# Kernel tuning notes

Hardware: AMD Instinct MI355X
Metric: run time of the kernel (lower is better)

The kernel has to match this reference:

```python
import jax, jax.numpy as jnp
import numpy as np

H = 128        # hidden_dim
NP = 512       # program nodes
NV = 50000     # voxel nodes
E = 800000     # cross edges (16 per voxel)
TAU = 1.0
SLOPE = 0.01   # LeakyReLU default negative slope


def setup_inputs() -> dict:
    key = jax.random.key(0)
    ks = jax.random.split(key, 12)
    s = 1.0 / np.sqrt(H)
    x = jax.random.normal(ks[0], (NP, H), dtype=jnp.float32)
    v = jax.random.normal(ks[1], (NV, H), dtype=jnp.float32)
    row0 = jax.random.randint(ks[2], (E,), 0, NP, dtype=jnp.int32)
    row1 = (jnp.arange(E, dtype=jnp.int32) % NV)  # every voxel gets E/NV edges
    cross_edge_index = jnp.stack([row0, row1])    # [2, E]
    W_program = jax.random.normal(ks[3], (H, H), dtype=jnp.float32) * s
    b_program = jnp.zeros((H,), dtype=jnp.float32)
    W_voxel = jax.random.normal(ks[4], (H, H), dtype=jnp.float32) * s
    b_voxel = jnp.zeros((H,), dtype=jnp.float32)
    W_m1 = jax.random.normal(ks[5], (H, H), dtype=jnp.float32) * s
    b_m1 = jnp.zeros((H,), dtype=jnp.float32)
    W_m2 = jax.random.normal(ks[6], (H, 1), dtype=jnp.float32) * s
    b_m2 = jnp.zeros((1,), dtype=jnp.float32)
    theta = jax.random.normal(ks[7], (H, 1), dtype=jnp.float32) * s  # xavier-like
    u = jax.random.uniform(ks[8], (E,), dtype=jnp.float32)
    gumbel_u = jnp.clip(u, 1e-7, 1.0 - 1e-7)  # avoid log(0)
    return {"x": x, "v": v, "cross_edge_index": cross_edge_index,
            "W_program": W_program, "b_program": b_program,
            "W_voxel": W_voxel, "b_voxel": b_voxel,
            "W_m1": W_m1, "b_m1": b_m1, "W_m2": W_m2, "b_m2": b_m2,
            "theta": theta, "gumbel_u": gumbel_u}


def reference(x, v, cross_edge_index, W_program, b_program, W_voxel, b_voxel,
              W_m1, b_m1, W_m2, b_m2, theta, gumbel_u):
    src = cross_edge_index[0]
    dst = cross_edge_index[1]
    x_sel = x[src]                      # [E, H] gather
    v_sel = v[dst]                      # [E, H] gather
    # mask = sigmoid(MLP(v)) : Linear -> LeakyReLU -> Linear(H,1)
    a = v @ W_m1 + b_m1
    a = jnp.where(a >= 0, a, SLOPE * a)
    mask = jax.nn.sigmoid(a @ W_m2 + b_m2)                  # [NV, 1]
    # attention logits: theta^T * tanh(Wp x_sel + Wv v_sel), summed over H
    t = jnp.tanh(x_sel @ W_program + b_program + v_sel @ W_voxel + b_voxel)
    e = jnp.sum(t * theta[:, 0], axis=-1)                   # [E]
    # Gumbel softmax: global softmax over all edges (dim=0 in torch on 1-D e)
    g = -jnp.log(-jnp.log(gumbel_u))
    y = jax.nn.softmax((e + g) / TAU)                       # [E]
    # per-voxel hard argmax (scatter_max), straight-through estimator
    seg_max = jax.ops.segment_max(y, dst, num_segments=NV)  # [NV]
    is_max = y == seg_max[dst]
    cand = jnp.where(is_max, jnp.arange(E), E)
    argmax = jax.ops.segment_min(cand, dst, num_segments=NV)  # [NV], first max per voxel
    y_hard_1 = jnp.zeros(E + 1, y.dtype).at[argmax].set(1.0)[:E]  # overflow slot for empty segments
    y_hard = jax.lax.stop_gradient(y_hard_1 - y) + y
    # scatter-sum of soft-attended program features back to voxels
    summed = jax.ops.segment_sum(x_sel * y[:, None], dst, num_segments=NV)  # [NV, H]
    v_out = v + mask * summed
    return (v_out, mask, y[:, None], y_hard[:, None])
```

## Files before the change

### kernel.cpp

```cpp
#include <hip/hip_runtime.h>

#define H     128
#define NP    512
#define NVOX  50000
#define NEDGE 800000
#define EPV   16
#define SLOPE 0.01f
#define GR    32
#define NBLK  ((NVOX + GR - 1) / GR)
#define STRH  136
#define VSTR  132
#define C1    2.8853900817779268f
#define LOG2E 1.4426950408889634f
#define LN2   0.6931471805599453f

#define EXP2(x) __builtin_amdgcn_exp2f(x)
#define LOG2(x) __builtin_amdgcn_logf(x)
#define RCP(x)  __builtin_amdgcn_rcpf(x)

typedef _Float16 h16;
typedef __attribute__((ext_vector_type(4))) _Float16 h16x4;
typedef __attribute__((ext_vector_type(8))) _Float16 h16x8;
typedef __attribute__((ext_vector_type(4))) float    f32x4;

__global__ __launch_bounds__(256) void k_pre(const float* __restrict__ x,
                                             const float* __restrict__ Wp,
                                             const float* __restrict__ bp,
                                             const float* __restrict__ Wv,
                                             const float* __restrict__ Wm1,
                                             float* __restrict__ xpout,
                                             h16* __restrict__ WvThi,
                                             h16* __restrict__ WvTlo,
                                             h16* __restrict__ Wm1T) {
    __shared__ float part[H];
    int bid = blockIdx.x;
    int tid = threadIdx.x;
    if (bid < NP) {
        int row = bid;
        int col = tid & 127;
        int kh  = tid >> 7;
        int kbase = kh * 64;
        const float* xr = x + (size_t)row * H;
        float acc = 0.f;
#pragma unroll 8
        for (int k = 0; k < 64; ++k)
            acc = fmaf(xr[kbase + k], Wp[(size_t)(kbase + k) * H + col], acc);
        if (kh == 1) part[col] = acc;
        __syncthreads();
        if (kh == 0) xpout[(size_t)row * H + col] = (acc + part[col] + bp[col]) * C1;
    } else {
        int idx = (bid - NP) * 256 + tid;
        if (idx < 16384) {
            int k = idx >> 7, n = idx & 127;
            float w = Wv[idx];
            h16 hi = (h16)w;
            WvThi[n * H + k] = hi;
            WvTlo[n * H + k] = (h16)(w - (float)hi);
        } else {
            int j = idx - 16384;
            int k = j >> 7, n = j & 127;
            Wm1T[n * H + k] = (h16)Wm1[j];
        }
    }
}

__global__ __launch_bounds__(256) void k_main(
    const float* __restrict__ v,
    const float* __restrict__ bv,  const float* __restrict__ bm1,
    const float* __restrict__ Wm2, const float* __restrict__ bm2,
    const h16* __restrict__ WvThi, const h16* __restrict__ WvTlo,
    const h16* __restrict__ Wm1T,
    const float* __restrict__ xp,  const int* __restrict__ cei,
    const float* __restrict__ theta, const float* __restrict__ gum,
    float* __restrict__ mask_out, float* __restrict__ pout,
    float* __restrict__ partial)
{
    __shared__ __align__(16) char ldsbuf[GR * STRH * 2 * 2];
    h16*   vh = (h16*)ldsbuf;
    h16*   vl = vh + GR * STRH;
    float* vt = (float*)ldsbuf;
    __shared__ float pmbuf[4][GR];
    __shared__ float psums[4];

    int tid  = threadIdx.x;
    int base = blockIdx.x * GR;

#pragma unroll
    for (int i = 0; i < 4; ++i) {
        int f  = i * 256 + tid;
        int r  = f >> 5, c4 = f & 31;
        int gr = base + r;
        float4 val = (gr < NVOX) ? *(const float4*)&v[(size_t)gr * H + c4 * 4]
                                 : make_float4(0.f, 0.f, 0.f, 0.f);
        h16x4 hi, lo;
        hi.x = (h16)val.x; lo.x = (h16)(val.x - (float)hi.x);
        hi.y = (h16)val.y; lo.y = (h16)(val.y - (float)hi.y);
        hi.z = (h16)val.z; lo.z = (h16)(val.z - (float)hi.z);
        hi.w = (h16)val.w; lo.w = (h16)(val.w - (float)hi.w);
        *(h16x4*)&vh[r * STRH + c4 * 4] = hi;
        *(h16x4*)&vl[r * STRH + c4 * 4] = lo;
    }
    __syncthreads();

    int wave = tid >> 6, lane = tid & 63;
    int m16 = lane & 15, quad = lane >> 4;
    int cb = wave * 32;

    f32x4 aV[2][2], aM[2][2];
#pragma unroll
    for (int rt = 0; rt < 2; ++rt)
#pragma unroll
        for (int ct = 0; ct < 2; ++ct) { aV[rt][ct] = (f32x4)0.f; aM[rt][ct] = (f32x4)0.f; }

#pragma unroll
    for (int kc = 0; kc < 4; ++kc) {
        int kofs = kc * 32 + quad * 8;
        h16x8 ah[2], al[2];
#pragma unroll
        for (int rt = 0; rt < 2; ++rt) {
            int row = rt * 16 + m16;
            ah[rt] = *(const h16x8*)&vh[row * STRH + kofs];
            al[rt] = *(const h16x8*)&vl[row * STRH + kofs];
        }
#pragma unroll
        for (int ct = 0; ct < 2; ++ct) {
            int n = cb + ct * 16 + m16;
            h16x8 bh = *(const h16x8*)&WvThi[n * H + kofs];
            h16x8 bl = *(const h16x8*)&WvTlo[n * H + kofs];
            h16x8 bm = *(const h16x8*)&Wm1T[n * H + kofs];
#pragma unroll
            for (int rt = 0; rt < 2; ++rt) {
                aV[rt][ct] = __builtin_amdgcn_mfma_f32_16x16x32_f16(ah[rt], bh, aV[rt][ct], 0, 0, 0);
                aV[rt][ct] = __builtin_amdgcn_mfma_f32_16x16x32_f16(al[rt], bh, aV[rt][ct], 0, 0, 0);
                aV[rt][ct] = __builtin_amdgcn_mfma_f32_16x16x32_f16(ah[rt], bl, aV[rt][ct], 0, 0, 0);
                aM[rt][ct] = __builtin_amdgcn_mfma_f32_16x16x32_f16(ah[rt], bm, aM[rt][ct], 0, 0, 0);
            }
        }
    }
    __syncthreads();

    float pml[2][4];
#pragma unroll
    for (int rt = 0; rt < 2; ++rt)
#pragma unroll
        for (int reg = 0; reg < 4; ++reg) pml[rt][reg] = 0.f;
#pragma unroll
    for (int ct = 0; ct < 2; ++ct) {
        int col = cb + ct * 16 + m16;
        float bvc = bv[col], bmc = bm1[col], w2c = Wm2[col];
#pragma unroll
        for (int rt = 0; rt < 2; ++rt)
#pragma unroll
            for (int reg = 0; reg < 4; ++reg) {
                int row = rt * 16 + quad * 4 + reg;
                vt[row * VSTR + col] = (aV[rt][ct][reg] + bvc) * C1;
                float m = aM[rt][ct][reg] + bmc;
                m = (m >= 0.f) ? m : SLOPE * m;
                pml[rt][reg] = fmaf(m, w2c, pml[rt][reg]);
            }
    }
#pragma unroll
    for (int off = 8; off >= 1; off >>= 1)
#pragma unroll
        for (int rt = 0; rt < 2; ++rt)
#pragma unroll
            for (int reg = 0; reg < 4; ++reg)
                pml[rt][reg] += __shfl_xor(pml[rt][reg], off, 64);
    if (m16 == 0) {
#pragma unroll
        for (int rt = 0; rt < 2; ++rt)
#pragma unroll
            for (int reg = 0; reg < 4; ++reg)
                pmbuf[wave][rt * 16 + quad * 4 + reg] = pml[rt][reg];
    }
    __syncthreads();
    if (wave == 0 && lane < GR) {
        int gr = base + lane;
        if (gr < NVOX) {
            float s = pmbuf[0][lane] + pmbuf[1][lane] + pmbuf[2][lane]
                    + pmbuf[3][lane] + bm2[0];
            mask_out[gr] = RCP(1.f + EXP2(-s * LOG2E));
        }
    }

    int g = tid >> 3, lk = tid & 7;
    float th2[16], thsum = 0.f;
#pragma unroll
    for (int i = 0; i < 4; ++i) {
        float4 t4 = *(const float4*)&theta[(lk + 8 * i) * 4];
        th2[i * 4 + 0] = -2.f * t4.x; th2[i * 4 + 1] = -2.f * t4.y;
        th2[i * 4 + 2] = -2.f * t4.z; th2[i * 4 + 3] = -2.f * t4.w;
        thsum += t4.x + t4.y + t4.z + t4.w;
    }
    int vox = base + g;
    bool valid = vox < NVOX;
    const float* vr = &vt[g * VSTR];
    float4 b0 = *(const float4*)&vr[(lk +  0) * 4];
    float4 b1 = *(const float4*)&vr[(lk +  8) * 4];
    float4 b2 = *(const float4*)&vr[(lk + 16) * 4];
    float4 b3 = *(const float4*)&vr[(lk + 24) * 4];

    float psum = 0.f;
    for (int t = 0; t < EPV; ++t) {
        int e   = vox + t * NVOX;
        int src = valid ? cei[e] : 0;
        const float4* xr = (const float4*)(xp + (size_t)src * H);
        float4 a0 = xr[lk], a1 = xr[lk + 8], a2 = xr[lk + 16], a3 = xr[lk + 24];
        float acc0 = thsum, acc1 = 0.f;
        acc0 = fmaf(th2[ 0], RCP(EXP2(a0.x + b0.x) + 1.f), acc0);
        acc1 = fmaf(th2[ 1], RCP(EXP2(a0.y + b0.y) + 1.f), acc1);
        acc0 = fmaf(th2[ 2], RCP(EXP2(a0.z + b0.z) + 1.f), acc0);
        acc1 = fmaf(th2[ 3], RCP(EXP2(a0.w + b0.w) + 1.f), acc1);
        acc0 = fmaf(th2[ 4], RCP(EXP2(a1.x + b1.x) + 1.f), acc0);
        acc1 = fmaf(th2[ 5], RCP(EXP2(a1.y + b1.y) + 1.f), acc1);
        acc0 = fmaf(th2[ 6], RCP(EXP2(a1.z + b1.z) + 1.f), acc0);
        acc1 = fmaf(th2[ 7], RCP(EXP2(a1.w + b1.w) + 1.f), acc1);
        acc0 = fmaf(th2[ 8], RCP(EXP2(a2.x + b2.x) + 1.f), acc0);
        acc1 = fmaf(th2[ 9], RCP(EXP2(a2.y + b2.y) + 1.f), acc1);
        acc0 = fmaf(th2[10], RCP(EXP2(a2.z + b2.z) + 1.f), acc0);
        acc1 = fmaf(th2[11], RCP(EXP2(a2.w + b2.w) + 1.f), acc1);
        acc0 = fmaf(th2[12], RCP(EXP2(a3.x + b3.x) + 1.f), acc0);
        acc1 = fmaf(th2[13], RCP(EXP2(a3.y + b3.y) + 1.f), acc1);
        acc0 = fmaf(th2[14], RCP(EXP2(a3.z + b3.z) + 1.f), acc0);
        acc1 = fmaf(th2[15], RCP(EXP2(a3.w + b3.w) + 1.f), acc1);
        float acc = acc0 + acc1;
        acc += __shfl_xor(acc, 4, 64);
        acc += __shfl_xor(acc, 2, 64);
        acc += __shfl_xor(acc, 1, 64);
        if (lk == 0 && valid) {
            float u  = gum[e];
            float l1 = LOG2(u);
            float t1 = -LN2 * l1;
            float gm = -LN2 * LOG2(t1);
            float p  = EXP2((acc + gm) * LOG2E);
            pout[e] = p;
            psum   += p;
        }
    }
#pragma unroll
    for (int off = 32; off >= 1; off >>= 1) psum += __shfl_xor(psum, off, 64);
    __syncthreads();
    if (lane == 0) psums[wave] = psum;
    __syncthreads();
    if (tid == 0)
        partial[blockIdx.x] = psums[0] + psums[1] + psums[2] + psums[3];
}

__global__ __launch_bounds__(256) void k_reduce(const float* __restrict__ partial,
                                                float* __restrict__ invS) {
    __shared__ float wsum[4];
    int tid = threadIdx.x;
    float s = 0.f;
    for (int i = tid; i < NBLK; i += 256) s += partial[i];
#pragma unroll
    for (int off = 32; off >= 1; off >>= 1) s += __shfl_xor(s, off, 64);
    if ((tid & 63) == 0) wsum[tid >> 6] = s;
    __syncthreads();
    if (tid == 0) invS[0] = 1.f / (wsum[0] + wsum[1] + wsum[2] + wsum[3]);
}

__global__ __launch_bounds__(256) void k_out(const float* __restrict__ v,
                                             const float* __restrict__ x,
                                             const int* __restrict__ cei,
                                             const float* __restrict__ maskp,
                                             const float* __restrict__ invSp,
                                             float* __restrict__ vout,
                                             float* __restrict__ ybuf,
                                             float* __restrict__ yhard) {
    __shared__ float yt[EPV][32];
    __shared__ int   st[EPV][32];
    __shared__ int   am[32];
    int tid  = threadIdx.x;
    int base = blockIdx.x * 32;
    float invS = invSp[0];
#pragma unroll
    for (int it = 0; it < 2; ++it) {
        int idx = it * 256 + tid;
        int t = idx >> 5, c = idx & 31;
        int vox = base + c;
        if (vox < NVOX) {
            int e = vox + t * NVOX;
            float y = ybuf[e] * invS;
            yt[t][c] = y;
            st[t][c] = cei[e];
            ybuf[e]  = y;
        }
    }
    __syncthreads();
    if (tid < 32 && base + tid < NVOX) {
        int c = tid;
        float mx = yt[0][c]; int a = 0;
#pragma unroll
        for (int t = 1; t < EPV; ++t) {
            float yv = yt[t][c];
            if (yv > mx) { mx = yv; a = t; }
        }
        am[c] = a;
    }
    __syncthreads();
#pragma unroll
    for (int it = 0; it < 2; ++it) {
        int idx = it * 256 + tid;
        int t = idx >> 5, c = idx & 31;
        int vox = base + c;
        if (vox < NVOX) yhard[vox + t * NVOX] = (t == am[c]) ? 1.f : 0.f;
    }
    int c4 = (tid & 31) * 4;
    for (int vx = tid >> 5; vx < 32; vx += 8) {
        int vox = base + vx;
        if (vox >= NVOX) break;
        float4 acc = make_float4(0.f, 0.f, 0.f, 0.f);
#pragma unroll
        for (int t = 0; t < EPV; ++t) {
            float y = yt[t][vx];
            const float4 xv = *(const float4*)&x[(size_t)st[t][vx] * H + c4];
            acc.x = fmaf(y, xv.x, acc.x);
            acc.y = fmaf(y, xv.y, acc.y);
            acc.z = fmaf(y, xv.z, acc.z);
            acc.w = fmaf(y, xv.w, acc.w);
        }
        float m = maskp[vox];
        const float4 vv = *(const float4*)&v[(size_t)vox * H + c4];
        float4 o;
        o.x = fmaf(m, acc.x, vv.x);
        o.y = fmaf(m, acc.y, vv.y);
        o.z = fmaf(m, acc.z, vv.z);
        o.w = fmaf(m, acc.w, vv.w);
        *(float4*)&vout[(size_t)vox * H + c4] = o;
    }
}

extern "C" void kernel_launch(void* const* d_in, const int* in_sizes, int n_in,
                              void* d_out, int out_size, void* d_ws, size_t ws_size,
                              hipStream_t stream) {
    (void)in_sizes; (void)n_in; (void)out_size; (void)ws_size;
    const float* x   = (const float*)d_in[0];
    const float* v   = (const float*)d_in[1];
    const int*   cei = (const int*)d_in[2];
    const float* Wp  = (const float*)d_in[3];
    const float* bp  = (const float*)d_in[4];
    const float* Wv  = (const float*)d_in[5];
    const float* bv  = (const float*)d_in[6];
    const float* Wm1 = (const float*)d_in[7];
    const float* bm1 = (const float*)d_in[8];
    const float* Wm2 = (const float*)d_in[9];
    const float* bm2 = (const float*)d_in[10];
    const float* th  = (const float*)d_in[11];
    const float* gum = (const float*)d_in[12];

    float* out   = (float*)d_out;
    float* vout  = out;
    float* maskp = out + (size_t)NVOX * H;
    float* ybuf  = maskp + NVOX;
    float* yhard = ybuf + NEDGE;
    float* xp      = yhard;
    float* partial = yhard + 65536;
    h16*   WvThi   = (h16*)(yhard + 67104);
    h16*   WvTlo   = WvThi + 16384;
    h16*   Wm1T    = WvThi + 32768;
    float* invS    = (float*)d_ws;

    k_pre<<<NP + 128, 256, 0, stream>>>(x, Wp, bp, Wv, Wm1, xp, WvThi, WvTlo, Wm1T);
    k_main<<<NBLK, 256, 0, stream>>>(v, bv, bm1, Wm2, bm2, WvThi, WvTlo, Wm1T,
                                     xp, cei, th, gum, maskp, ybuf, partial);
    k_reduce<<<1, 256, 0, stream>>>(partial, invS);
    k_out<<<(NVOX + 31) / 32, 256, 0, stream>>>(v, x, cei, maskp, invS, vout, ybuf, yhard);
}
```

Baseline: 187.7 us.

## Fuse soft-attended scatter-sum and argmax into main edge kernel, merge reduce into output

The main kernel now gathers the raw x rows alongside the precomputed projections and accumulates the unnormalised weighted sum per voxel in registers, writing it into the output buffer. It also computes the per-voxel argmax and marks it by storing the negated probability. The separate reduce kernel is removed: every output block redoes the small partial-sum reduction, then rescales either v_out or y/y_hard elementwise. This removes the second gather of x and cei in the output pass and one kernel launch, in exchange for extra gather traffic and register pressure in the main loop, plus a redundant reduction in each output block.

```diff
diff --git a/kernel.cpp b/kernel.cpp
--- a/kernel.cpp
+++ b/kernel.cpp
@@ -13,6 +13,7 @@
 #define C1    2.8853900817779268f
 #define LOG2E 1.4426950408889634f
 #define LN2   0.6931471805599453f
+#define ABLK  3125
 
 #define EXP2(x) __builtin_amdgcn_exp2f(x)
 #define LOG2(x) __builtin_amdgcn_logf(x)
@@ -64,8 +65,8 @@
     }
 }
 
-__global__ __launch_bounds__(256) void k_main(
-    const float* __restrict__ v,
+__global__ __launch_bounds__(256, 2) void k_main(
+    const float* __restrict__ v,   const float* __restrict__ x,
     const float* __restrict__ bv,  const float* __restrict__ bm1,
     const float* __restrict__ Wm2, const float* __restrict__ bm2,
     const h16* __restrict__ WvThi, const h16* __restrict__ WvTlo,
@@ -73,7 +74,7 @@
     const float* __restrict__ xp,  const int* __restrict__ cei,
     const float* __restrict__ theta, const float* __restrict__ gum,
     float* __restrict__ mask_out, float* __restrict__ pout,
-    float* __restrict__ partial)
+    float* __restrict__ sump,     float* __restrict__ partial)
 {
     __shared__ __align__(16) char ldsbuf[GR * STRH * 2 * 2];
     h16*   vh = (h16*)ldsbuf;
@@ -81,6 +82,8 @@
     float* vt = (float*)ldsbuf;
     __shared__ float pmbuf[4][GR];
     __shared__ float psums[4];
+    __shared__ float ptile[EPV][GR];
+    __shared__ int   amtile[GR];
 
     int tid  = threadIdx.x;
     int base = blockIdx.x * GR;
@@ -200,12 +203,17 @@
     float4 b2 = *(const float4*)&vr[(lk + 16) * 4];
     float4 b3 = *(const float4*)&vr[(lk + 24) * 4];
 
-    float psum = 0.f;
+    float4 s0 = make_float4(0.f,0.f,0.f,0.f), s1 = s0, s2 = s0, s3 = s0;
+    float psum = 0.f, pmax = -1.f;
+    int   pidx = 0;
+#pragma unroll 2
     for (int t = 0; t < EPV; ++t) {
         int e   = vox + t * NVOX;
         int src = valid ? cei[e] : 0;
         const float4* xr = (const float4*)(xp + (size_t)src * H);
+        const float4* xo = (const float4*)(x  + (size_t)src * H);
         float4 a0 = xr[lk], a1 = xr[lk + 8], a2 = xr[lk + 16], a3 = xr[lk + 24];
+        float4 c0 = xo[lk], c1 = xo[lk + 8], c2 = xo[lk + 16], c3 = xo[lk + 24];
         float acc0 = thsum, acc1 = 0.f;
         acc0 = fmaf(th2[ 0], RCP(EXP2(a0.x + b0.x) + 1.f), acc0);
         acc1 = fmaf(th2[ 1], RCP(EXP2(a0.y + b0.y) + 1.f), acc1);
@@ -227,106 +235,81 @@
         acc += __shfl_xor(acc, 4, 64);
         acc += __shfl_xor(acc, 2, 64);
         acc += __shfl_xor(acc, 1, 64);
-        if (lk == 0 && valid) {
-            float u  = gum[e];
-            float l1 = LOG2(u);
-            float t1 = -LN2 * l1;
-            float gm = -LN2 * LOG2(t1);
-            float p  = EXP2((acc + gm) * LOG2E);
-            pout[e] = p;
-            psum   += p;
+        float u  = gum[valid ? e : 0];
+        float gm = -LN2 * LOG2(-LN2 * LOG2(u));
+        float p  = EXP2((acc + gm) * LOG2E);
+        if (p > pmax) { pmax = p; pidx = t; }
+        psum += (lk == 0 && valid) ? p : 0.f;
+        if (lk == 0) ptile[t][g] = p;
+        s0.x = fmaf(p, c0.x, s0.x); s0.y = fmaf(p, c0.y, s0.y);
+        s0.z = fmaf(p, c0.z, s0.z); s0.w = fmaf(p, c0.w, s0.w);
+        s1.x = fmaf(p, c1.x, s1.x); s1.y = fmaf(p, c1.y, s1.y);
+        s1.z = fmaf(p, c1.z, s1.z); s1.w = fmaf(p, c1.w, s1.w);
+        s2.x = fmaf(p, c2.x, s2.x); s2.y = fmaf(p, c2.y, s2.y);
+        s2.z = fmaf(p, c2.z, s2.z); s2.w = fmaf(p, c2.w, s2.w);
+        s3.x = fmaf(p, c3.x, s3.x); s3.y = fmaf(p, c3.y, s3.y);
+        s3.z = fmaf(p, c3.z, s3.z); s3.w = fmaf(p, c3.w, s3.w);
+    }
+    if (lk == 0) amtile[g] = pidx;
+    if (valid) {
+        float* sr = sump + (size_t)vox * H;
+        *(float4*)&sr[(lk +  0) * 4] = s0;
+        *(float4*)&sr[(lk +  8) * 4] = s1;
+        *(float4*)&sr[(lk + 16) * 4] = s2;
+        *(float4*)&sr[(lk + 24) * 4] = s3;
+    }
+    __syncthreads();
+#pragma unroll
+    for (int it = 0; it < 2; ++it) {
+        int t = (tid >> 5) + 8 * it, c = tid & 31;
+        int vox2 = base + c;
+        if (vox2 < NVOX) {
+            float val = ptile[t][c];
+            pout[vox2 + t * NVOX] = (t == amtile[c]) ? -val : val;
         }
     }
 #pragma unroll
     for (int off = 32; off >= 1; off >>= 1) psum += __shfl_xor(psum, off, 64);
-    __syncthreads();
     if (lane == 0) psums[wave] = psum;
     __syncthreads();
     if (tid == 0)
         partial[blockIdx.x] = psums[0] + psums[1] + psums[2] + psums[3];
 }
 
-__global__ __launch_bounds__(256) void k_reduce(const float* __restrict__ partial,
-                                                float* __restrict__ invS) {
-    __shared__ float wsum[4];
+__global__ __launch_bounds__(256) void k_out(const float* __restrict__ v,
+                                             const float* __restrict__ maskp,
+                                             const float* __restrict__ partial,
+                                             float* __restrict__ vout,
+                                             float* __restrict__ ybuf,
+                                             float* __restrict__ yhard) {
+    __shared__ float red[4];
     int tid = threadIdx.x;
     float s = 0.f;
     for (int i = tid; i < NBLK; i += 256) s += partial[i];
 #pragma unroll
     for (int off = 32; off >= 1; off >>= 1) s += __shfl_xor(s, off, 64);
-    if ((tid & 63) == 0) wsum[tid >> 6] = s;
-    __syncthreads();
-    if (tid == 0) invS[0] = 1.f / (wsum[0] + wsum[1] + wsum[2] + wsum[3]);
-}
-
-__global__ __launch_bounds__(256) void k_out(const float* __restrict__ v,
-                                             const float* __restrict__ x,
-                                             const int* __restrict__ cei,
-                                             const float* __restrict__ maskp,
-                                             const float* __restrict__ invSp,
-                                             float* __restrict__ vout,
-                                             float* __restrict__ ybuf,
-                                             float* __restrict__ yhard) {
-    __shared__ float yt[EPV][32];
-    __shared__ int   st[EPV][32];
-    __shared__ int   am[32];
-    int tid  = threadIdx.x;
-    int base = blockIdx.x * 32;
-    float invS = invSp[0];
-#pragma unroll
-    for (int it = 0; it < 2; ++it) {
-        int idx = it * 256 + tid;
-        int t = idx >> 5, c = idx & 31;
-        int vox = base + c;
-        if (vox < NVOX) {
-            int e = vox + t * NVOX;
-            float y = ybuf[e] * invS;
-            yt[t][c] = y;
-            st[t][c] = cei[e];
-            ybuf[e]  = y;
-        }
-    }
-    __syncthreads();
-    if (tid < 32 && base + tid < NVOX) {
-        int c = tid;
-        float mx = yt[0][c]; int a = 0;
-#pragma unroll
-        for (int t = 1; t < EPV; ++t) {
-            float yv = yt[t][c];
-            if (yv > mx) { mx = yv; a = t; }
-        }
-        am[c] = a;
-    }
-    __syncthreads();
-#pragma unroll
-    for (int it = 0; it < 2; ++it) {
-        int idx = it * 256 + tid;
-        int t = idx >> 5, c = idx & 31;
-        int vox = base + c;
-        if (vox < NVOX) yhard[vox + t * NVOX] = (t == am[c]) ? 1.f : 0.f;
-    }
-    int c4 = (tid & 31) * 4;
-    for (int vx = tid >> 5; vx < 32; vx += 8) {
-        int vox = base + vx;
-        if (vox >= NVOX) break;
-        float4 acc = make_float4(0.f, 0.f, 0.f, 0.f);
-#pragma unroll
-        for (int t = 0; t < EPV; ++t) {
-            float y = yt[t][vx];
-            const float4 xv = *(const float4*)&x[(size_t)st[t][vx] * H + c4];
-            acc.x = fmaf(y, xv.x, acc.x);
-            acc.y = fmaf(y, xv.y, acc.y);
-            acc.z = fmaf(y, xv.z, acc.z);
-            acc.w = fmaf(y, xv.w, acc.w);
-        }
-        float m = maskp[vox];
-        const float4 vv = *(const float4*)&v[(size_t)vox * H + c4];
-        float4 o;
-        o.x = fmaf(m, acc.x, vv.x);
-        o.y = fmaf(m, acc.y, vv.y);
-        o.z = fmaf(m, acc.z, vv.z);
-        o.w = fmaf(m, acc.w, vv.w);
-        *(float4*)&vout[(size_t)vox * H + c4] = o;
+    if ((tid & 63) == 0) red[tid >> 6] = s;
+    __syncthreads();
+    float invS = RCP(red[0] + red[1] + red[2] + red[3]);
+
+    int bid = blockIdx.x;
+    if (bid < ABLK) {
+#pragma unroll
+        for (int r = 0; r < 2; ++r) {
+            int i = (bid + r * ABLK) * 256 + tid;
+            float4 sp = ((const float4*)vout)[i];
+            float4 vv = ((const float4*)v)[i];
+            float  m  = maskp[i >> 5] * invS;
+            float4 o;
+            o.x = fmaf(m, sp.x, vv.x); o.y = fmaf(m, sp.y, vv.y);
+            o.z = fmaf(m, sp.z, vv.z); o.w = fmaf(m, sp.w, vv.w);
+            ((float4*)vout)[i] = o;
+        }
+    } else {
+        int e = (bid - ABLK) * 256 + tid;
+        float pv = ybuf[e];
+        ybuf[e]  = fabsf(pv) * invS;
+        yhard[e] = (pv < 0.f) ? 1.f : 0.f;
     }
 }
 
@@ -353,16 +336,14 @@
     float* maskp = out + (size_t)NVOX * H;
     float* ybuf  = maskp + NVOX;
     float* yhard = ybuf + NEDGE;
-    float* xp      = yhard;
-    float* partial = yhard + 65536;
-    h16*   WvThi   = (h16*)(yhard + 67104);
-    h16*   WvTlo   = WvThi + 16384;
-    h16*   Wm1T    = WvThi + 32768;
-    float* invS    = (float*)d_ws;
+    float* xp    = yhard;
+    h16*   WvThi = (h16*)(yhard + 65536);
+    h16*   WvTlo = WvThi + 16384;
+    h16*   Wm1T  = WvThi + 32768;
+    float* partial = (float*)d_ws;
 
     k_pre<<<NP + 128, 256, 0, stream>>>(x, Wp, bp, Wv, Wm1, xp, WvThi, WvTlo, Wm1T);
-    k_main<<<NBLK, 256, 0, stream>>>(v, bv, bm1, Wm2, bm2, WvThi, WvTlo, Wm1T,
-                                     xp, cei, th, gum, maskp, ybuf, partial);
-    k_reduce<<<1, 256, 0, stream>>>(partial, invS);
-    k_out<<<(NVOX + 31) / 32, 256, 0, stream>>>(v, x, cei, maskp, invS, vout, ybuf, yhard);
+    k_main<<<NBLK, 256, 0, stream>>>(v, x, bv, bm1, Wm2, bm2, WvThi, WvTlo, Wm1T,
+                                     xp, cei, th, gum, maskp, ybuf, vout, partial);
+    k_out<<<2 * ABLK, 256, 0, stream>>>(v, maskp, partial, vout, ybuf, yhard);
 }
```

Measured after the change: 192.5 us. 1.03x slower.
